# Kernel optimization log

Measured on AMD Instinct MI355X. Metric: run time of the kernel, lower is better.

The kernel has to match this reference:

```python
import jax, jax.numpy as jnp
import numpy as np

CHEB_K = 2; HORIZON = 12; HFS = 4; D_HEAD = 32; EPS = 1e-5

def layer_norm(x, g, b):
    mu = x.mean(-1, keepdims=True)
    v = ((x - mu) ** 2).mean(-1, keepdims=True)
    return (x - mu) * jax.lax.rsqrt(v + EPS) * g + b

def gconv(x, supports, W, b):
    # x:[B,N,C], supports:[K,N,N], W:[N,K,C,O], b:[N,O]
    xg = jnp.einsum('knm,bmc->bnkc', supports, x)
    return jnp.einsum('bnkc,nkco->bno', xg, W) + b

def run_layer(x, state0, supports, gW, gb, uW, ub):
    # x:[B,T,N,C] -> hidden states [B,T,N,H] via GRU-style adaptive graph-conv recurrence
    def step(state, xt):
        xs = jnp.concatenate([xt, state], -1)
        zr = jax.nn.sigmoid(gconv(xs, supports, gW, gb))
        z, r = jnp.split(zr, 2, -1)
        hc = jnp.tanh(gconv(jnp.concatenate([xt, z * state], -1), supports, uW, ub))
        h = r * state + (1.0 - r) * hc
        return h, h
    _, hs = jax.lax.scan(step, state0, x.transpose(1, 0, 2, 3))
    return hs.transpose(1, 0, 2, 3)

def setup_inputs():
    key = jax.random.key(0)
    B, T, N, Din, H, E = 32, 12, 512, 2, 64, 16
    ks = iter(jax.random.split(key, 40))
    def rn(shape, scale):
        return jax.random.normal(next(ks), shape, jnp.float32) * scale
    inp = {}
    inp['source'] = rn((B, T, N, Din), 1.0)
    inp['targets'] = rn((B, T, N, 1), 1.0)
    inp['node_emb'] = rn((N, E), 1.0)
    for l, din in enumerate([Din, H]):
        c = din + H
        inp['gate_wpool_%d' % l] = rn((E, CHEB_K, c, 2 * H), (E * CHEB_K * c) ** -0.5)
        inp['gate_bpool_%d' % l] = rn((E, 2 * H), E ** -0.5)
        inp['upd_wpool_%d' % l] = rn((E, CHEB_K, c, H), (E * CHEB_K * c) ** -0.5)
        inp['upd_bpool_%d' % l] = rn((E, H), E ** -0.5)
    hyp_in = CHEB_K * H * CHEB_K * H
    inp['hyp_W'] = rn((hyp_in, HORIZON * HFS), hyp_in ** -0.5)
    inp['hyp_b'] = rn((HORIZON * HFS,), 0.02)
    for nm in ['Wq', 'Wk', 'Wv', 'ffW1', 'ffW2']:
        inp[nm] = rn((H, H), H ** -0.5)
    for nm in ['bq', 'bk', 'bv', 'ffb1', 'ffb2']:
        inp[nm] = jnp.zeros((H,), jnp.float32)
    inp['ln1_g'] = jnp.ones((H,), jnp.float32); inp['ln1_b'] = jnp.zeros((H,), jnp.float32)
    inp['ln2_g'] = jnp.ones((H,), jnp.float32); inp['ln2_b'] = jnp.zeros((H,), jnp.float32)
    inp['fc_W'] = rn((H, 1), H ** -0.5)
    inp['fc_b'] = jnp.zeros((1,), jnp.float32)
    return inp

def reference(source, targets, node_emb, gate_wpool_0, gate_bpool_0, upd_wpool_0, upd_bpool_0,
              gate_wpool_1, gate_bpool_1, upd_wpool_1, upd_bpool_1, hyp_W, hyp_b,
              Wq, bq, Wk, bk, Wv, bv, ln1_g, ln1_b, ffW1, ffb1, ffW2, ffb2, ln2_g, ln2_b, fc_W, fc_b):
    B, T, N, _ = source.shape
    H = Wq.shape[0]
    # adaptive supports (cheb_k = 2): [I, softmax(relu(E @ E^T), dim=1)]
    adj = jax.nn.softmax(jax.nn.relu(node_emb @ node_emb.T), axis=1)
    supports = jnp.stack([jnp.eye(N, dtype=source.dtype), adj], 0)  # [K,N,N]
    state0 = jnp.zeros((B, N, H), source.dtype)
    out = source
    for (gwp, gbp, uwp, ubp) in [(gate_wpool_0, gate_bpool_0, upd_wpool_0, upd_bpool_0),
                                 (gate_wpool_1, gate_bpool_1, upd_wpool_1, upd_bpool_1)]:
        gW = jnp.einsum('ne,ekio->nkio', node_emb, gwp); gb = node_emb @ gbp
        uW = jnp.einsum('ne,ekio->nkio', node_emb, uwp); ub = node_emb @ ubp
        out = run_layer(out, state0, supports, gW, gb, uW, ub)
        last_uW = uW  # encoder returns last layer's candidate-gconv per-node weights
    # Hypernetwork: dilation=0 grouped 1xHFS conv == scale last hidden state by sum of filter taps
    hlin = last_uW.reshape(N, -1) @ hyp_W + hyp_b               # [N, horizon*HFS]
    fs = hlin.reshape(N, HORIZON, HFS).sum(-1)                  # [N, horizon]
    h = jnp.einsum('bnh,nt->btnh', out[:, -1], fs)              # [B, horizon, N, H]
    # Transform attention block (L = 1; loop re-uses same `out`, only last iter matters)
    heads = H // D_HEAD
    q = out @ Wq + bq; k = out @ Wk + bk; v = h @ Wv + bv
    def split_heads(t):
        return t.reshape(B, T, N, heads, D_HEAD).transpose(3, 0, 2, 1, 4)  # [h,B,N,T,d]
    q, k, v = split_heads(q), split_heads(k), split_heads(v)
    A = jax.nn.softmax(jnp.einsum('hbntd,hbnsd->hbnts', q, k) / (D_HEAD ** 0.5), axis=-1)
    o = jnp.einsum('hbnts,hbnsd->hbntd', A, v)
    o = o.transpose(1, 3, 2, 0, 4).reshape(B, T, N, H)
    val = layer_norm(o + out, ln1_g, ln1_b)
    ffo = jnp.maximum(val @ ffW1 + ffb1, 0.0) @ ffW2 + ffb2
    out_h = layer_norm(ffo + val, ln2_g, ln2_b)
    y = (out_h @ fc_W + fc_b)[..., 0]                           # [B,T,N]
    y = y.reshape(-1, HORIZON, 1, N).transpose(0, 1, 3, 2)      # [B,horizon,N,1]
    return y
```

## Files before the change

### kernel.cpp

```cpp
#include <hip/hip_runtime.h>
#include <hip/hip_bf16.h>


using bf16 = __hip_bfloat16;
#define B2F(x) __bfloat162float(x)

#define NN 512
#define BBATCH 32
#define HHID 64
#define TT 12
#define EE 16

typedef __attribute__((ext_vector_type(4))) float f32x4;
typedef __attribute__((ext_vector_type(8))) short bf16x8;

__device__ inline float wsum(float x) {
#pragma unroll
  for (int off = 32; off > 0; off >>= 1) x += __shfl_xor(x, off, 64);
  return x;
}

__device__ inline uint4 llc_load4(const void* p) {
  uint4 r;
  asm volatile("global_load_dwordx4 %0, %1, off sc0 sc1" : "=v"(r) : "v"(p));
  return r;
}
__device__ inline uint4 cch_load4(const void* p) {
  uint4 r;
  asm volatile("global_load_dwordx4 %0, %1, off" : "=v"(r) : "v"(p));
  return r;
}
__device__ inline uint2 llc_load2(const void* p) {
  uint2 r;
  asm volatile("global_load_dwordx2 %0, %1, off sc0 sc1" : "=v"(r) : "v"(p));
  return r;
}
__device__ inline unsigned llc_load1(const void* p) {
  unsigned r;
  asm volatile("global_load_dword %0, %1, off sc0 sc1" : "=v"(r) : "v"(p));
  return r;
}
__device__ inline void llc_store_bf(void* p, unsigned short v) {
  asm volatile("global_store_short %0, %1, off sc0 sc1" :: "v"(p), "v"((unsigned)v) : "memory");
}
__device__ inline void llc_store_u1(void* p, unsigned v) {
  asm volatile("global_store_dword %0, %1, off sc0 sc1" :: "v"(p), "v"(v) : "memory");
}
template <int N> __device__ inline void wait_vmcnt() {
  if constexpr (N <= 0)      asm volatile("s_waitcnt vmcnt(0)" ::: "memory");
  else if constexpr (N == 1) asm volatile("s_waitcnt vmcnt(1)" ::: "memory");
  else if constexpr (N == 2) asm volatile("s_waitcnt vmcnt(2)" ::: "memory");
  else if constexpr (N == 3) asm volatile("s_waitcnt vmcnt(3)" ::: "memory");
  else if constexpr (N == 4) asm volatile("s_waitcnt vmcnt(4)" ::: "memory");
  else if constexpr (N == 5) asm volatile("s_waitcnt vmcnt(5)" ::: "memory");
  else if constexpr (N == 6) asm volatile("s_waitcnt vmcnt(6)" ::: "memory");
  else if constexpr (N == 7) asm volatile("s_waitcnt vmcnt(7)" ::: "memory");
  else if constexpr (N == 8) asm volatile("s_waitcnt vmcnt(8)" ::: "memory");
  else if constexpr (N == 10) asm volatile("s_waitcnt vmcnt(10)" ::: "memory");
  else if constexpr (N == 12) asm volatile("s_waitcnt vmcnt(12)" ::: "memory");
  else                       asm volatile("s_waitcnt vmcnt(14)" ::: "memory");
}

__device__ inline void lds_barrier() {
  asm volatile("s_waitcnt lgkmcnt(0)" ::: "memory");
  __builtin_amdgcn_s_barrier();
  asm volatile("" ::: "memory");
}

__device__ inline void gbar(unsigned* __restrict__ bar, int& cnt) {
  cnt++;
  __syncthreads();
  unsigned tgt = (unsigned)cnt;
  unsigned* flags = bar + 32;
  if (blockIdx.x == 0) {
    if (threadIdx.x < 64) {
      if (threadIdx.x == 0) llc_store_u1(flags, tgt);
      const unsigned* fp = flags + threadIdx.x * 8;
      bool ok;
      do {
        unsigned v0 = llc_load1(fp + 0), v1 = llc_load1(fp + 1),
                 v2 = llc_load1(fp + 2), v3 = llc_load1(fp + 3),
                 v4 = llc_load1(fp + 4), v5 = llc_load1(fp + 5),
                 v6 = llc_load1(fp + 6), v7 = llc_load1(fp + 7);
        wait_vmcnt<0>();
        __builtin_amdgcn_sched_barrier(0);
        ok = ((int)(v0 - tgt) >= 0) && ((int)(v1 - tgt) >= 0) &&
             ((int)(v2 - tgt) >= 0) && ((int)(v3 - tgt) >= 0) &&
             ((int)(v4 - tgt) >= 0) && ((int)(v5 - tgt) >= 0) &&
             ((int)(v6 - tgt) >= 0) && ((int)(v7 - tgt) >= 0);
      } while (!__all(ok));
      if (threadIdx.x == 0) llc_store_u1(bar, tgt);
    }
  } else if (threadIdx.x == 0) {
    llc_store_u1(flags + blockIdx.x, tgt);
    for (;;) {
      unsigned e = llc_load1(bar);
      wait_vmcnt<0>();
      __builtin_amdgcn_sched_barrier(0);
      if ((int)(e - tgt) >= 0) break;
      __builtin_amdgcn_s_sleep(2);
    }
  }
  __syncthreads();
}

__global__ __launch_bounds__(256) void zero_f32_kernel(float* __restrict__ p, int n) {
  int i = blockIdx.x * 256 + threadIdx.x;
  if (i < n) p[i] = 0.0f;
}


__global__ __launch_bounds__(256) void adj_kernel(const float* __restrict__ emb,
                                                  bf16* __restrict__ adjb) {
  __shared__ float embAll[NN * EE];
  __shared__ float red[256];
  int tid = threadIdx.x, n = blockIdx.x;
  for (int i = tid; i < NN * EE; i += 256) embAll[i] = emb[i];
  __syncthreads();
  float v[2];
#pragma unroll
  for (int j = 0; j < 2; j++) {
    int m = tid + j * 256;
    float s = 0.f;
#pragma unroll
    for (int e = 0; e < EE; e++) s += embAll[n * EE + e] * embAll[m * EE + e];
    v[j] = fmaxf(s, 0.0f);
  }
  float mx = fmaxf(v[0], v[1]);
  red[tid] = mx; __syncthreads();
  for (int s = 128; s > 0; s >>= 1) { if (tid < s) red[tid] = fmaxf(red[tid], red[tid + s]); __syncthreads(); }
  mx = red[0]; __syncthreads();
  float e0 = expf(v[0] - mx), e1 = expf(v[1] - mx);
  red[tid] = e0 + e1; __syncthreads();
  for (int s = 128; s > 0; s >>= 1) { if (tid < s) red[tid] += red[tid + s]; __syncthreads(); }
  float inv = 1.0f / red[0];
  adjb[n * NN + tid] = __float2bfloat16(e0 * inv);
  adjb[n * NN + tid + 256] = __float2bfloat16(e1 * inv);
}

__global__ __launch_bounds__(256) void wgen_kernel(const float* __restrict__ pool,
                                                   const float* __restrict__ emb,
                                                   float* __restrict__ out, int J) {
  __shared__ float embL[128 * EE];
  int tid = threadIdx.x;
  int n0 = blockIdx.y * 128;
  for (int i = tid; i < 128 * EE; i += 256) embL[i] = emb[n0 * EE + i];
  __syncthreads();
  int j = blockIdx.x * 256 + tid;
  if (j >= J) return;
  float pw[EE];
#pragma unroll
  for (int e = 0; e < EE; e++) pw[e] = pool[e * J + j];
#pragma unroll 4
  for (int nn = 0; nn < 128; nn++) {
    float s = 0.f;
#pragma unroll
    for (int e = 0; e < EE; e++) s += embL[nn * EE + e] * pw[e];
    out[(size_t)(n0 + nn) * J + j] = s;
  }
}

__global__ __launch_bounds__(256) void wgen_t_kernel(const float* __restrict__ pool,
                                                     const float* __restrict__ emb,
                                                     bf16* __restrict__ out, int J,
                                                     int O, int KCP, int KC) {
  __shared__ float embL[128 * EE];
  int tid = threadIdx.x;
  int n0 = blockIdx.y * 128;
  for (int i = tid; i < 128 * EE; i += 256) embL[i] = emb[n0 * EE + i];
  __syncthreads();
  int p = blockIdx.x * 256 + tid;
  unsigned kc = (unsigned)p % (unsigned)KCP;
  unsigned o = (unsigned)p / (unsigned)KCP;
  size_t P = (size_t)KCP * O;
  if (kc >= (unsigned)KC) {
    bf16 z = __float2bfloat16(0.f);
    for (int nn = 0; nn < 128; nn++) out[(size_t)(n0 + nn) * P + p] = z;
    return;
  }
  int jp = (int)kc * O + (int)o;
  float pw[EE];
#pragma unroll
  for (int e = 0; e < EE; e++) pw[e] = pool[e * J + jp];
#pragma unroll 4
  for (int nn = 0; nn < 128; nn++) {
    float s = 0.f;
#pragma unroll
    for (int e = 0; e < EE; e++) s += embL[nn * EE + e] * pw[e];
    out[(size_t)(n0 + nn) * P + p] = __float2bfloat16(s);
  }
}

__global__ __launch_bounds__(256) void hypwT_kernel(const float* __restrict__ hypW,
                                                    float* __restrict__ hypWT) {
  __shared__ float tile[48 * 33];
  int r0 = blockIdx.x * 32, tid = threadIdx.x;
  for (int i = tid; i < 32 * 48; i += 256) {
    int r = i / 48, c = i - r * 48;
    tile[c * 33 + r] = hypW[(size_t)(r0 + r) * 48 + c];
  }
  __syncthreads();
  for (int i = tid; i < 48 * 32; i += 256) {
    int c = i >> 5, r = i & 31;
    hypWT[(size_t)c * 16384 + r0 + r] = tile[c * 33 + r];
  }
}

__global__ __launch_bounds__(256) void pw_kernel(const float* __restrict__ upool,
                                                 const float* __restrict__ hypWT,
                                                 float* __restrict__ PW) {
  __shared__ float red[256];
  int j = blockIdx.x, e = blockIdx.y, tid = threadIdx.x;
  float s = 0.f;
#pragma unroll 4
  for (int p = tid; p < 16384; p += 256)
    s += upool[e * 16384 + p] * hypWT[(size_t)j * 16384 + p];
  red[tid] = s; __syncthreads();
  for (int t = 128; t > 0; t >>= 1) { if (tid < t) red[tid] += red[tid + t]; __syncthreads(); }
  if (tid == 0) PW[e * 48 + j] = red[0];
}

__global__ __launch_bounds__(256) void fs_kernel(const float* __restrict__ emb,
                                                 const float* __restrict__ PW,
                                                 const float* __restrict__ hypb,
                                                 float* __restrict__ fs) {
  int id = blockIdx.x * 256 + threadIdx.x;
  if (id >= NN * TT) return;
  int n = id / TT, t = id % TT;
  float s = 0.f;
#pragma unroll
  for (int f = 0; f < 4; f++) {
    int j = t * 4 + f;
    float h = hypb[j];
#pragma unroll
    for (int e = 0; e < EE; e++) h += emb[n * EE + e] * PW[e * 48 + j];
    s += h;
  }
  fs[id] = s;
}

__global__ __launch_bounds__(256) void cvt_src_kernel(const float* __restrict__ src,
                                                      bf16* __restrict__ x) {
  int id = blockIdx.x * 256 + threadIdx.x;
  int c = id & 1, b = (id >> 1) & 31, n = (id >> 6) & 511, t = id >> 15;
  x[id] = __float2bfloat16(src[((b * TT + t) * NN + n) * 2 + c]);
}

#define DBUF 4672

__device__ inline void xsT_wr8(unsigned short* xsT, int base, int q0l, int k, uint4 v) {
  union { uint4 u; unsigned short h[8]; } cv; cv.u = v;
#pragma unroll
  for (int qq = 0; qq < 8; qq++) {
    int q = q0l + qq;
    xsT[base + q * 72 + (q >> 3) * 8 + k] = cv.h[qq];
  }
}

#define DIFF_STEP(cc)                                                         \
  {                                                                           \
    if constexpr ((cc) < 7) {                                                 \
      wait_vmcnt<(6 - (cc)) * LPC>();                                         \
      constexpr int nb = ((((cc) + 1) & 1)) * DBUF;                           \
      xsT_wr8(xsT, nb, ql, kr, pre[((cc) + 1) & 7][0]);                       \
      if constexpr (QW == 64)                                                 \
        xsT_wr8(xsT, nb, ql, 32 + kr, pre[((cc) + 1) & 7][1]);                \
    }                                                                         \
    constexpr int base = ((cc) & 1) * DBUF;                                   \
    _Pragma("unroll")                                                         \
    for (int ki = 0; ki < 2; ki++) {                                          \
      bf16x8 a = apre[(cc) * 2 + ki];                                         \
      _Pragma("unroll")                                                       \
      for (int ct = 0; ct < NCT; ct++) {                                      \
        int q = ct * 16 + col;                                                \
        bf16x8 b = *(const bf16x8*)&xsT[base + q * 72 + (q >> 3) * 8 +        \
                                        ki * 32 + quad * 8];                  \
        acc[ct] = __builtin_amdgcn_mfma_f32_16x16x32_bf16(a, b, acc[ct], 0, 0, 0); \
      }                                                                       \
    }                                                                         \
    lds_barrier();                                                            \
  }

template <int QW, bool CACHED>
__device__ inline void diffuse_tileP(const bf16x8* __restrict__ apre,
                                     const bf16* __restrict__ X, bf16* __restrict__ Y,
                                     int Q, int n0, int q0, char* smraw, int tid) {
  constexpr int LPC = QW / 32;
  constexpr int NCT = QW / 16;
  unsigned short* xsT = (unsigned short*)smraw;
  int w = tid >> 6, lane = tid & 63;
  int col = lane & 15, quad = lane >> 4;
  int kr, ql;
  if constexpr (QW == 64) { kr = tid >> 3; ql = (tid & 7) * 8; }
  else                    { kr = tid >> 2; ql = (tid & 3) * 8; }
  f32x4 acc[NCT];
#pragma unroll
  for (int ct = 0; ct < NCT; ct++) acc[ct] = (f32x4){0.f, 0.f, 0.f, 0.f};
  const bf16* Xb = X + q0 + ql;
  uint4 pre[8][LPC];
#pragma unroll
  for (int c = 0; c < 8; c++) {
    if constexpr (CACHED) {
      pre[c][0] = cch_load4(Xb + (size_t)(c * 64 + kr) * Q);
      if constexpr (QW == 64)
        pre[c][1] = cch_load4(Xb + (size_t)(c * 64 + 32 + kr) * Q);
    } else {
      pre[c][0] = llc_load4(Xb + (size_t)(c * 64 + kr) * Q);
      if constexpr (QW == 64)
        pre[c][1] = llc_load4(Xb + (size_t)(c * 64 + 32 + kr) * Q);
    }
  }
  wait_vmcnt<7 * LPC>();
  xsT_wr8(xsT, 0, ql, kr, pre[0][0]);
  if constexpr (QW == 64) xsT_wr8(xsT, 0, ql, 32 + kr, pre[0][1]);
  lds_barrier();
  DIFF_STEP(0) DIFF_STEP(1) DIFF_STEP(2) DIFF_STEP(3)
  DIFF_STEP(4) DIFF_STEP(5) DIFF_STEP(6) DIFF_STEP(7)
#pragma unroll
  for (int ct = 0; ct < NCT; ct++)
#pragma unroll
    for (int r = 0; r < 4; r++) {
      int row = n0 + w * 16 + quad * 4 + r;
      bf16 hb = __float2bfloat16(acc[ct][r]);
      llc_store_bf(Y + (size_t)row * Q + q0 + ct * 16 + col, *(unsigned short*)&hb);
    }
}


template <int C>
__device__ inline void stage_A(int n, int tid, unsigned short* xinb,
    const bf16* __restrict__ xt, const bf16* __restrict__ xd,
    const bf16* __restrict__ sa, const bf16* __restrict__ sad) {
  constexpr int cc = C + HHID, KC = 2 * cc, KCP = (KC + 31) & ~31, PIT = KCP + 8;
  __syncthreads();
  for (int i = tid; i < 32 * KCP; i += 256) {
    int b = i / KCP, kc = i - b * KCP;
    unsigned short v = 0;
    if (kc < C)            v = *(const unsigned short*)&xt[(n * 32 + b) * C + kc];
    else if (kc < cc)      v = *(const unsigned short*)&sa[(n * 32 + b) * HHID + kc - C];
    else if (kc < cc + C)  v = *(const unsigned short*)&xd[(n * 32 + b) * C + kc - cc];
    else if (kc < KC)      v = *(const unsigned short*)&sad[(n * 32 + b) * HHID + kc - cc - C];
    xinb[b * PIT + kc] = v;
  }
  __syncthreads();
}

template <int C>
__device__ inline void gate_epilogue(int n, int w, int col, int quad,
    f32x4 acc[2][2], const float* __restrict__ gb, const float* __restrict__ state,
    bf16* __restrict__ zs, bf16* __restrict__ rbuf) {
#pragma unroll
  for (int i = 0; i < 2; i++) {
    int o = (w + i * 4) * 16 + col;
    float bv = gb[n * 128 + o];
#pragma unroll
    for (int mt = 0; mt < 2; mt++)
#pragma unroll
      for (int r = 0; r < 4; r++) {
        int m = mt * 16 + quad * 4 + r;
        float zr = 1.0f / (1.0f + expf(-(acc[i][mt][r] + bv)));
        int idx = (n * 32 + m) * HHID + (o & 63);
        if (o < HHID) zs[idx] = __float2bfloat16(zr * state[idx]);
        else          rbuf[idx] = __float2bfloat16(zr);
      }
  }
}

template <int C>
__device__ inline void upd_epilogue(int n, int w, int col, int quad,
    f32x4 acc[2], const float* __restrict__ ub, float* __restrict__ state,
    bf16* __restrict__ sb, const bf16* __restrict__ rbuf, bf16* __restrict__ xo) {
  int o = w * 16 + col;
  float bv = ub[n * 64 + o];
#pragma unroll
  for (int mt = 0; mt < 2; mt++)
#pragma unroll
    for (int r = 0; r < 4; r++) {
      int m = mt * 16 + quad * 4 + r;
      int idx = (n * 32 + m) * HHID + o;
      float hc = tanhf(acc[mt][r] + bv);
      float rr = B2F(rbuf[idx]);
      float st = state[idx];
      float h = rr * st + (1.0f - rr) * hc;
      state[idx] = h;
      bf16 hb = __float2bfloat16(h);
      sb[idx] = hb;
      xo[idx] = hb;
    }
}

template <int C>
__device__ inline void gate_mfma(int n, int tid, const unsigned short* xinb,
    const bf16* __restrict__ gWt, const float* __restrict__ gb,
    const float* __restrict__ state, bf16* __restrict__ zs, bf16* __restrict__ rbuf) {
  constexpr int KC = 2 * (C + HHID), KCP = (KC + 31) & ~31, PIT = KCP + 8;
  int w = tid >> 6, lane = tid & 63, col = lane & 15, quad = lane >> 4;
  f32x4 acc[2][2];
#pragma unroll
  for (int i = 0; i < 2; i++)
#pragma unroll
    for (int mt = 0; mt < 2; mt++) acc[i][mt] = (f32x4){0.f, 0.f, 0.f, 0.f};
  const bf16* Wn = gWt + (size_t)n * KCP * 128;
#pragma unroll 2
  for (int k0 = 0; k0 < KCP; k0 += 32) {
    int ko = k0 + quad * 8;
    bf16x8 a0 = *(const bf16x8*)&xinb[col * PIT + ko];
    bf16x8 a1 = *(const bf16x8*)&xinb[(16 + col) * PIT + ko];
#pragma unroll
    for (int i = 0; i < 2; i++) {
      int o = (w + i * 4) * 16 + col;
      bf16x8 bf = *(const bf16x8*)(Wn + (size_t)o * KCP + ko);
      acc[i][0] = __builtin_amdgcn_mfma_f32_16x16x32_bf16(a0, bf, acc[i][0], 0, 0, 0);
      acc[i][1] = __builtin_amdgcn_mfma_f32_16x16x32_bf16(a1, bf, acc[i][1], 0, 0, 0);
    }
  }
  gate_epilogue<C>(n, w, col, quad, acc, gb, state, zs, rbuf);
}

template <int C>
__device__ inline void upd_mfma(int n, int tid, const unsigned short* xinb,
    const bf16* __restrict__ uWt, const float* __restrict__ ub,
    float* __restrict__ state, bf16* __restrict__ sb,
    const bf16* __restrict__ rbuf, bf16* __restrict__ xo) {
  constexpr int KC = 2 * (C + HHID), KCP = (KC + 31) & ~31, PIT = KCP + 8;
  int w = tid >> 6, lane = tid & 63, col = lane & 15, quad = lane >> 4;
  f32x4 acc[2];
  acc[0] = (f32x4){0.f, 0.f, 0.f, 0.f};
  acc[1] = (f32x4){0.f, 0.f, 0.f, 0.f};
  const bf16* Wn = uWt + (size_t)n * KCP * 64;
  int o = w * 16 + col;
#pragma unroll 2
  for (int k0 = 0; k0 < KCP; k0 += 32) {
    int ko = k0 + quad * 8;
    bf16x8 a0 = *(const bf16x8*)&xinb[col * PIT + ko];
    bf16x8 a1 = *(const bf16x8*)&xinb[(16 + col) * PIT + ko];
    bf16x8 bf = *(const bf16x8*)(Wn + (size_t)o * KCP + ko);
    acc[0] = __builtin_amdgcn_mfma_f32_16x16x32_bf16(a0, bf, acc[0], 0, 0, 0);
    acc[1] = __builtin_amdgcn_mfma_f32_16x16x32_bf16(a1, bf, acc[1], 0, 0, 0);
  }
  upd_epilogue<C>(n, w, col, quad, acc, ub, state, sb, rbuf, xo);
}


template <int C>
__global__ __launch_bounds__(256, 2) void recur_kernel(
    const bf16* __restrict__ adjb, const bf16* __restrict__ xin,
    const bf16* __restrict__ gWt, const float* __restrict__ gb,
    const bf16* __restrict__ uWt, const float* __restrict__ ub,
    bf16* __restrict__ zsAll, bf16* __restrict__ sdiff, bf16* __restrict__ zsdiff,
    bf16* __restrict__ xd, bf16* __restrict__ xout, unsigned* __restrict__ bar) {
  constexpr int KC = 2 * (C + HHID), KCP = (KC + 31) & ~31, PIT = KCP + 8;
  constexpr int NK = KCP / 32;
  constexpr int QX = 32 * C;
  __shared__ __align__(16) char dsm[2 * DBUF * 2];
  __shared__ __align__(16) unsigned short xinb[32 * PIT];
  int bid = blockIdx.x, tid = threadIdx.x;
  int w = tid >> 6, lane = tid & 63, col = lane & 15, quad = lane >> 4;
  int bcnt = 0;

  bf16x8 apre[16];
  {
    int n0p = ((bid & 255) >> 5) * 64;
    const bf16* ar = adjb + (size_t)(n0p + w * 16 + col) * NN;
#pragma unroll
    for (int c = 0; c < 8; c++)
#pragma unroll
      for (int ki = 0; ki < 2; ki++)
        apre[c * 2 + ki] = *(const bf16x8*)(ar + c * 64 + ki * 32 + quad * 8);
  }
  bf16x8 fg[2 * NK];
  {
    const bf16* Wn = gWt + (size_t)bid * KCP * 128;
#pragma unroll
    for (int i = 0; i < 2; i++) {
      int o = (w + i * 4) * 16 + col;
#pragma unroll
      for (int kk = 0; kk < NK; kk++)
        fg[i * NK + kk] = *(const bf16x8*)(Wn + (size_t)o * KCP + kk * 32 + quad * 8);
    }
  }
  bf16x8 fu[NK];
  {
    const bf16* Wn = uWt + (size_t)bid * KCP * 64;
    int o = w * 16 + col;
#pragma unroll
    for (int kk = 0; kk < NK; kk++)
      fu[kk] = *(const bf16x8*)(Wn + (size_t)o * KCP + kk * 32 + quad * 8);
  }
  float gbv0 = gb[bid * 128 + w * 16 + col];
  float gbv1 = gb[bid * 128 + 64 + w * 16 + col];
  float ubv  = ub[bid * 64 + w * 16 + col];

  for (int i = tid; i < 32 * PIT; i += 256) xinb[i] = 0;
  __syncthreads();

  int r2 = tid >> 3, ch = tid & 7;
  uint4 vxt; unsigned sxt = 0, sxd = 0;
  if constexpr (C == 64) {
    vxt = *(const uint4*)(xin + (size_t)(bid * 32 + r2) * 64 + ch * 8);
  } else {
    if (tid < 32) sxt = *(const unsigned*)(xin + (size_t)(bid * 32 + tid) * 2);
  }

  float st[2][4], rr_[2][4];
#pragma unroll
  for (int mt = 0; mt < 2; mt++)
#pragma unroll
    for (int r4 = 0; r4 < 4; r4++) st[mt][r4] = 0.f;

  if constexpr (C == 2) {
    int wg = (bid & 31) | ((bid >> 8) << 5);
    if (wg < TT)
      diffuse_tileP<64, true>(apre, xin + (size_t)wg * NN * QX,
                              xd + (size_t)wg * NN * QX, QX,
                              ((bid & 255) >> 5) * 64, 0, dsm, tid);
  } else {
    if (bid >= 256)
      diffuse_tileP<64, true>(apre, xin, xd, 2048, ((bid & 255) >> 5) * 64,
                              (bid & 31) * 64, dsm, tid);
  }
  gbar(bar, bcnt);

  for (int t = 0; t < TT; t++) {
    const bf16* xt = xin + (size_t)t * NN * QX;
    const bf16* xdt = (C == 2) ? (xd + (size_t)t * NN * QX) : xd;
    bf16* xo = xout + (size_t)t * NN * 32 * HHID;
    bf16* zst = zsAll + (size_t)t * NN * 32 * HHID;
    if (t > 0) {
      const bf16* sbp = xout + (size_t)(t - 1) * NN * 32 * HHID;
      if constexpr (C == 64) {
        if (bid < 256)
          diffuse_tileP<64, true>(apre, sbp, sdiff, 2048, (bid >> 5) * 64,
                                  (bid & 31) * 64, dsm, tid);
        else
          diffuse_tileP<64, true>(apre, xt, xd, 2048, ((bid & 255) >> 5) * 64,
                                  (bid & 31) * 64, dsm, tid);
      } else {
        int cs = (bid & 31) | ((bid >> 8) << 5);
        diffuse_tileP<32, true>(apre, sbp, sdiff, 2048, ((bid & 255) >> 5) * 64,
                                cs * 32, dsm, tid);
      }
      gbar(bar, bcnt);
    }
    if constexpr (C == 64) {
      *(uint4*)&xinb[r2 * PIT + ch * 8] = vxt;
      uint4 v1 = llc_load4(xdt + (size_t)(bid * 32 + r2) * 64 + ch * 8);
      uint4 v2;
      if (t > 0) v2 = llc_load4(sdiff + (size_t)(bid * 32 + r2) * 64 + ch * 8);
      wait_vmcnt<0>();
      *(uint4*)&xinb[r2 * PIT + 128 + ch * 8] = v1;
      if (t > 0) *(uint4*)&xinb[r2 * PIT + 192 + ch * 8] = v2;
    } else {
      if (tid < 32) *(unsigned*)&xinb[tid * PIT] = sxt;
      if (t == 0) {
        if (tid < 32) {
          unsigned v = llc_load1(xdt + (size_t)(bid * 32 + tid) * 2);
          wait_vmcnt<0>();
          *(unsigned*)&xinb[tid * PIT + 66] = v;
        }
      } else {
        if (tid >= 32 && tid < 64) *(unsigned*)&xinb[(tid - 32) * PIT + 66] = sxd;
        int r2a = tid >> 4, c4 = tid & 15;
        uint2 va = llc_load2(sdiff + (size_t)(bid * 32 + r2a) * 64 + c4 * 4);
        uint2 vb = llc_load2(sdiff + (size_t)(bid * 32 + 16 + r2a) * 64 + c4 * 4);
        wait_vmcnt<0>();
        *(uint2*)&xinb[r2a * PIT + 68 + c4 * 4] = va;
        *(uint2*)&xinb[(16 + r2a) * PIT + 68 + c4 * 4] = vb;
      }
    }
    __syncthreads();
    {
      f32x4 acc[2][2];
#pragma unroll
      for (int i = 0; i < 2; i++)
#pragma unroll
        for (int mt = 0; mt < 2; mt++) acc[i][mt] = (f32x4){0.f, 0.f, 0.f, 0.f};
#pragma unroll
      for (int kk = 0; kk < NK; kk++) {
        int ko = kk * 32 + quad * 8;
        bf16x8 a0 = *(const bf16x8*)&xinb[col * PIT + ko];
        bf16x8 a1 = *(const bf16x8*)&xinb[(16 + col) * PIT + ko];
#pragma unroll
        for (int i = 0; i < 2; i++) {
          acc[i][0] = __builtin_amdgcn_mfma_f32_16x16x32_bf16(a0, fg[i * NK + kk], acc[i][0], 0, 0, 0);
          acc[i][1] = __builtin_amdgcn_mfma_f32_16x16x32_bf16(a1, fg[i * NK + kk], acc[i][1], 0, 0, 0);
        }
      }
      __syncthreads();
#pragma unroll
      for (int mt = 0; mt < 2; mt++)
#pragma unroll
        for (int r4 = 0; r4 < 4; r4++) {
          int m = mt * 16 + quad * 4 + r4;
          float z = 1.0f / (1.0f + expf(-(acc[0][mt][r4] + gbv0)));
          float rv = 1.0f / (1.0f + expf(-(acc[1][mt][r4] + gbv1)));
          rr_[mt][r4] = rv;
          bf16 zb = __float2bfloat16(z * st[mt][r4]);
          xinb[m * PIT + C + w * 16 + col] = *(unsigned short*)&zb;
          llc_store_bf(zst + (size_t)(bid * 32 + m) * 64 + w * 16 + col,
                       *(unsigned short*)&zb);
        }
    }
    if (t > 0) {
      gbar(bar, bcnt);
      {
        int cs = (bid & 31) | ((bid >> 8) << 5);
        diffuse_tileP<32, true>(apre, zst, zsdiff, 2048, ((bid & 255) >> 5) * 64,
                                cs * 32, dsm, tid);
      }
      gbar(bar, bcnt);
      if constexpr (C == 64) {
        uint4 v = llc_load4(zsdiff + (size_t)(bid * 32 + r2) * 64 + ch * 8);
        wait_vmcnt<0>();
        *(uint4*)&xinb[r2 * PIT + 192 + ch * 8] = v;
      } else {
        int r2a = tid >> 4, c4 = tid & 15;
        uint2 va = llc_load2(zsdiff + (size_t)(bid * 32 + r2a) * 64 + c4 * 4);
        uint2 vb = llc_load2(zsdiff + (size_t)(bid * 32 + 16 + r2a) * 64 + c4 * 4);
        wait_vmcnt<0>();
        *(uint2*)&xinb[r2a * PIT + 68 + c4 * 4] = va;
        *(uint2*)&xinb[(16 + r2a) * PIT + 68 + c4 * 4] = vb;
      }
    }
    __syncthreads();
    {
      f32x4 acc[2];
      acc[0] = (f32x4){0.f, 0.f, 0.f, 0.f};
      acc[1] = (f32x4){0.f, 0.f, 0.f, 0.f};
#pragma unroll
      for (int kk = 0; kk < NK; kk++) {
        int ko = kk * 32 + quad * 8;
        bf16x8 a0 = *(const bf16x8*)&xinb[col * PIT + ko];
        bf16x8 a1 = *(const bf16x8*)&xinb[(16 + col) * PIT + ko];
        acc[0] = __builtin_amdgcn_mfma_f32_16x16x32_bf16(a0, fu[kk], acc[0], 0, 0, 0);
        acc[1] = __builtin_amdgcn_mfma_f32_16x16x32_bf16(a1, fu[kk], acc[1], 0, 0, 0);
      }
      __syncthreads();
      if (t + 1 < TT) {
        if constexpr (C == 64) {
          vxt = *(const uint4*)(xin + (size_t)(t + 1) * NN * QX +
                                (size_t)(bid * 32 + r2) * 64 + ch * 8);
        } else {
          if (tid < 32)
            sxt = *(const unsigned*)(xin + (size_t)(t + 1) * NN * QX +
                                     (size_t)(bid * 32 + tid) * 2);
          else if (tid < 64)
            sxd = *(const unsigned*)(xd + (size_t)(t + 1) * NN * QX +
                                     (size_t)(bid * 32 + (tid - 32)) * 2);
        }
      }
#pragma unroll
      for (int mt = 0; mt < 2; mt++)
#pragma unroll
        for (int r4 = 0; r4 < 4; r4++) {
          int m = mt * 16 + quad * 4 + r4;
          float hc = tanhf(acc[mt][r4] + ubv);
          float rv = rr_[mt][r4];
          float h = rv * st[mt][r4] + (1.0f - rv) * hc;
          st[mt][r4] = h;
          bf16 hb = __float2bfloat16(h);
          xinb[m * PIT + C + w * 16 + col] = *(unsigned short*)&hb;
          llc_store_bf(xo + (size_t)(bid * 32 + m) * 64 + w * 16 + col,
                       *(unsigned short*)&hb);
        }
    }
    gbar(bar, bcnt);
  }
}


__global__ __launch_bounds__(256, 2) void diffuse0_kernel(const bf16* __restrict__ adjb,
                                                          const bf16* __restrict__ X,
                                                          bf16* __restrict__ Y) {
  __shared__ __align__(16) char smraw[2 * DBUF * 2];
  int bid = blockIdx.x, tid = threadIdx.x;
  int t = bid >> 3, n0 = (bid & 7) * 64;
  int w = tid >> 6, lane = tid & 63, col = lane & 15, quad = lane >> 4;
  bf16x8 ap[16];
  const bf16* ar = adjb + (size_t)(n0 + w * 16 + col) * NN;
#pragma unroll
  for (int c = 0; c < 8; c++)
#pragma unroll
    for (int ki = 0; ki < 2; ki++)
      ap[c * 2 + ki] = *(const bf16x8*)(ar + c * 64 + ki * 32 + quad * 8);
  diffuse_tileP<64, true>(ap, X + (size_t)t * NN * 64, Y + (size_t)t * NN * 64,
                          64, n0, 0, smraw, tid);
}

__global__ __launch_bounds__(256, 2) void diffuse1_kernel(const bf16* __restrict__ adjb,
                                                          const bf16* __restrict__ X,
                                                          bf16* __restrict__ Y) {
  __shared__ __align__(16) char smraw[2 * DBUF * 2];
  int bid = blockIdx.x, tid = threadIdx.x;
  int n0 = (bid >> 5) * 64;
  int w = tid >> 6, lane = tid & 63, col = lane & 15, quad = lane >> 4;
  bf16x8 ap[16];
  const bf16* ar = adjb + (size_t)(n0 + w * 16 + col) * NN;
#pragma unroll
  for (int c = 0; c < 8; c++)
#pragma unroll
    for (int ki = 0; ki < 2; ki++)
      ap[c * 2 + ki] = *(const bf16x8*)(ar + c * 64 + ki * 32 + quad * 8);
  diffuse_tileP<64, true>(ap, X, Y, 2048, n0, (bid & 31) * 64, smraw, tid);
}

template <int C>
__global__ __launch_bounds__(256, 2) void gate_wrap(
    const bf16* xt, const bf16* xdt, const bf16* sa, const bf16* sad,
    const bf16* gWt, const float* gb, const float* state, bf16* zs, bf16* rbuf) {
  constexpr int KC = 2 * (C + HHID), KCP = (KC + 31) & ~31, PIT = KCP + 8;
  __shared__ __align__(16) unsigned short xinb[32 * PIT];
  stage_A<C>(blockIdx.x, threadIdx.x, xinb, xt, xdt, sa, sad);
  gate_mfma<C>(blockIdx.x, threadIdx.x, xinb, gWt, gb, state, zs, rbuf);
}

template <int C>
__global__ __launch_bounds__(256, 2) void upd_wrap(
    const bf16* xt, const bf16* xdt, const bf16* sa, const bf16* sad,
    const bf16* uWt, const float* ub, float* state, bf16* sb,
    const bf16* rbuf, bf16* xo) {
  constexpr int KC = 2 * (C + HHID), KCP = (KC + 31) & ~31, PIT = KCP + 8;
  __shared__ __align__(16) unsigned short xinb[32 * PIT];
  stage_A<C>(blockIdx.x, threadIdx.x, xinb, xt, xdt, sa, sad);
  upd_mfma<C>(blockIdx.x, threadIdx.x, xinb, uWt, ub, state, sb, rbuf, xo);
}


#define TP 68
#define WS 72

__global__ __launch_bounds__(256, 4) void attn1_kernel(
    const bf16* __restrict__ x1, const float* __restrict__ fsb,
    const float* __restrict__ Wq, const float* __restrict__ bq,
    const float* __restrict__ Wk, const float* __restrict__ bk,
    const float* __restrict__ Wv, const float* __restrict__ bv,
    const float* __restrict__ ln1g, const float* __restrict__ ln1b,
    bf16* __restrict__ val) {
  __shared__ bf16 WqT[WS * 64], WkT[WS * 64];
  __shared__ bf16 Wv_s[4096];
  __shared__ bf16 Xb[16 * 72];
  __shared__ float qs[TT * TP], ks[TT * TP];
  __shared__ float A[2 * TT * TT];
  __shared__ float ovv[64], fss[TT];
  __shared__ float bqs[64], bks[64], bvs[64], g1s[64], b1s[64];
  int tid = threadIdx.x;
  int w = tid >> 6, lane = tid & 63, col = lane & 15, quad = lane >> 4;
#pragma unroll
  for (int i = 0; i < 16; i++) {
    int e = tid * 16 + i;
    int hi = e >> 6, ho = e & 63;
    WqT[ho * WS + hi] = __float2bfloat16(Wq[e]);
    WkT[ho * WS + hi] = __float2bfloat16(Wk[e]);
  }
  for (int i = tid; i < 4096; i += 256) Wv_s[i] = __float2bfloat16(Wv[i]);
  for (int i = tid; i < 16 * 72; i += 256) Xb[i] = __float2bfloat16(0.f);
  if (tid < 64) {
    bqs[tid] = bq[tid]; bks[tid] = bk[tid]; bvs[tid] = bv[tid];
    g1s[tid] = ln1g[tid]; b1s[tid] = ln1b[tid];
  }
  __syncthreads();
  for (int g = 0; g < 8; g++) {
    int p = blockIdx.x * 8 + g;
    int b = p >> 9, n = p & 511;
    for (int i = tid; i < TT * 64; i += 256) {
      int t = i >> 6, j = i & 63;
      Xb[t * 72 + j] = x1[(((size_t)t * NN + n) * BBATCH + b) * HHID + j];
    }
    if (tid < TT) fss[tid] = fsb[n * TT + tid];
    __syncthreads();
    {
      f32x4 aq = (f32x4){0.f, 0.f, 0.f, 0.f};
      f32x4 ak = (f32x4){0.f, 0.f, 0.f, 0.f};
#pragma unroll
      for (int ki = 0; ki < 2; ki++) {
        bf16x8 af = *(const bf16x8*)&Xb[col * 72 + ki * 32 + quad * 8];
        bf16x8 bqf = *(const bf16x8*)&WqT[(w * 16 + col) * WS + ki * 32 + quad * 8];
        bf16x8 bkf = *(const bf16x8*)&WkT[(w * 16 + col) * WS + ki * 32 + quad * 8];
        aq = __builtin_amdgcn_mfma_f32_16x16x32_bf16(af, bqf, aq, 0, 0, 0);
        ak = __builtin_amdgcn_mfma_f32_16x16x32_bf16(af, bkf, ak, 0, 0, 0);
      }
#pragma unroll
      for (int r = 0; r < 4; r++) {
        int t = quad * 4 + r;
        if (t < TT) {
          int h = w * 16 + col;
          qs[t * TP + h] = aq[r] + bqs[h];
          ks[t * TP + h] = ak[r] + bks[h];
        }
      }
    }
    if (tid < 64) {
      float s = 0.f;
#pragma unroll 8
      for (int j = 0; j < 64; j++)
        s += B2F(Xb[11 * 72 + j]) * B2F(Wv_s[j * 64 + tid]);
      ovv[tid] = s;
    }
    __syncthreads();
    for (int i = tid; i < 2 * TT * TT; i += 256) {
      int hd = i / (TT * TT), ts = i % (TT * TT), t = ts / TT, s = ts % TT;
      float acc = 0.f;
#pragma unroll
      for (int d = 0; d < 32; d++) acc += qs[t * TP + hd * 32 + d] * ks[s * TP + hd * 32 + d];
      A[i] = acc * 0.17677669529663687f;
    }
    __syncthreads();
    if (tid < 2 * TT) {
      int hd = tid / TT, t = tid % TT;
      float* row = &A[hd * TT * TT + t * TT];
      float m = row[0];
      for (int s = 1; s < TT; s++) m = fmaxf(m, row[s]);
      float sm = 0.f;
      for (int s = 0; s < TT; s++) { float e = expf(row[s] - m); row[s] = e; sm += e; }
      float inv = 1.0f / sm;
      for (int s = 0; s < TT; s++) row[s] *= inv;
    }
    __syncthreads();
#pragma unroll
    for (int it = 0; it < 3; it++) {
      int i = it * 256 + tid;
      int t = i >> 6, h = i & 63, hd = h >> 5;
      float afs = 0.f;
#pragma unroll
      for (int s = 0; s < TT; s++) afs += A[hd * TT * TT + t * TT + s] * fss[s];
      float o = ovv[h] * afs + bvs[h];
      float x = o + B2F(Xb[t * 72 + h]);
      float mu = wsum(x) * (1.0f / 64.0f);
      float d = x - mu;
      float var = wsum(d * d) * (1.0f / 64.0f);
      float v = d * rsqrtf(var + 1e-5f) * g1s[h] + b1s[h];
      val[((size_t)(b * TT + t) * NN + n) * HHID + h] = __float2bfloat16(v);
    }
    __syncthreads();
  }
}

__global__ __launch_bounds__(256, 4) void ffn_kernel(
    const bf16* __restrict__ val, const float* __restrict__ W1, const float* __restrict__ b1,
    const float* __restrict__ W2, const float* __restrict__ b2,
    const float* __restrict__ ln2g, const float* __restrict__ ln2b,
    const float* __restrict__ fcW, const float* __restrict__ fcb,
    float* __restrict__ out, int rows_per_block) {
  __shared__ bf16 W1T[WS * 64], W2T[WS * 64];
  __shared__ bf16 Ab[16 * 72];
  __shared__ bf16 Hh[16 * 72], Hl[16 * 72];
  __shared__ float fout[16 * 68];
  __shared__ float b1s[64], b2s[64], g2s[64], bb2[64], fcs[64];
  int tid = threadIdx.x;
  int w = tid >> 6, lane = tid & 63, col = lane & 15, quad = lane >> 4;
#pragma unroll
  for (int i = 0; i < 16; i++) {
    int e = tid * 16 + i;
    int hi = e >> 6, ho = e & 63;
    W1T[ho * WS + hi] = __float2bfloat16(W1[e]);
    W2T[ho * WS + hi] = __float2bfloat16(W2[e]);
  }
  if (tid < 64) {
    b1s[tid] = b1[tid]; b2s[tid] = b2[tid];
    g2s[tid] = ln2g[tid]; bb2[tid] = ln2b[tid]; fcs[tid] = fcW[tid];
  }
  __syncthreads();
  float fcbv = fcb[0];
  for (int c0 = 0; c0 < rows_per_block; c0 += 16) {
    size_t r0 = (size_t)blockIdx.x * rows_per_block + c0;
    for (int i = tid; i < 1024; i += 256) {
      int rr = i >> 6, j = i & 63;
      Ab[rr * 72 + j] = val[(r0 + rr) * 64 + j];
    }
    __syncthreads();
    {
      f32x4 a1 = (f32x4){0.f, 0.f, 0.f, 0.f};
#pragma unroll
      for (int ki = 0; ki < 2; ki++) {
        bf16x8 af = *(const bf16x8*)&Ab[col * 72 + ki * 32 + quad * 8];
        bf16x8 bf1 = *(const bf16x8*)&W1T[(w * 16 + col) * WS + ki * 32 + quad * 8];
        a1 = __builtin_amdgcn_mfma_f32_16x16x32_bf16(af, bf1, a1, 0, 0, 0);
      }
#pragma unroll
      for (int r = 0; r < 4; r++) {
        int m = quad * 4 + r, h = w * 16 + col;
        float hv = fmaxf(a1[r] + b1s[h], 0.0f);
        bf16 hb = __float2bfloat16(hv);
        float lo = hv - B2F(hb);
        Hh[m * 72 + h] = hb;
        Hl[m * 72 + h] = __float2bfloat16(lo);
      }
    }
    __syncthreads();
    {
      f32x4 a2 = (f32x4){0.f, 0.f, 0.f, 0.f};
#pragma unroll
      for (int ki = 0; ki < 2; ki++) {
        bf16x8 ah = *(const bf16x8*)&Hh[col * 72 + ki * 32 + quad * 8];
        bf16x8 al = *(const bf16x8*)&Hl[col * 72 + ki * 32 + quad * 8];
        bf16x8 bf2 = *(const bf16x8*)&W2T[(w * 16 + col) * WS + ki * 32 + quad * 8];
        a2 = __builtin_amdgcn_mfma_f32_16x16x32_bf16(ah, bf2, a2, 0, 0, 0);
        a2 = __builtin_amdgcn_mfma_f32_16x16x32_bf16(al, bf2, a2, 0, 0, 0);
      }
#pragma unroll
      for (int r = 0; r < 4; r++) {
        int m = quad * 4 + r, h = w * 16 + col;
        fout[m * 68 + h] = a2[r] + b2s[h] + B2F(Ab[m * 72 + h]);
      }
    }
    __syncthreads();
#pragma unroll
    for (int p4 = 0; p4 < 4; p4++) {
      int m = p4 * 4 + w;
      float y = fout[m * 68 + lane];
      float mu = wsum(y) * (1.0f / 64.0f);
      float d = y - mu;
      float var = wsum(d * d) * (1.0f / 64.0f);
      float oh = d * rsqrtf(var + 1e-5f) * g2s[lane] + bb2[lane];
      float contrib = wsum(oh * fcs[lane]);
      if (lane == 0) out[r0 + m] = contrib + fcbv;
    }
    __syncthreads();
  }
}

extern "C" void kernel_launch(void* const* d_in, const int* in_sizes, int n_in,
                              void* d_out, int out_size, void* d_ws, size_t ws_size,
                              hipStream_t stream) {
  const float* src = (const float*)d_in[0];
  const float* emb = (const float*)d_in[2];
  const float* gwp[2] = {(const float*)d_in[3], (const float*)d_in[7]};
  const float* gbp[2] = {(const float*)d_in[4], (const float*)d_in[8]};
  const float* uwp[2] = {(const float*)d_in[5], (const float*)d_in[9]};
  const float* ubp[2] = {(const float*)d_in[6], (const float*)d_in[10]};
  const float* hypW = (const float*)d_in[11];
  const float* hypb = (const float*)d_in[12];
  const float *Wq, *Wk, *Wv, *ffW1, *ffW2, *bq, *bk, *bv, *ffb1, *ffb2;
  const float *ln1g, *ln1b, *ln2g, *ln2b, *fcW, *fcb;
  if (in_sizes[14] == 4096) {
    Wq = (const float*)d_in[13]; Wk = (const float*)d_in[14]; Wv = (const float*)d_in[15];
    ffW1 = (const float*)d_in[16]; ffW2 = (const float*)d_in[17];
    bq = (const float*)d_in[18]; bk = (const float*)d_in[19]; bv = (const float*)d_in[20];
    ffb1 = (const float*)d_in[21]; ffb2 = (const float*)d_in[22];
    ln1g = (const float*)d_in[23]; ln1b = (const float*)d_in[24];
    ln2g = (const float*)d_in[25]; ln2b = (const float*)d_in[26];
    fcW = (const float*)d_in[27]; fcb = (const float*)d_in[28];
  } else {
    Wq = (const float*)d_in[13]; bq = (const float*)d_in[14];
    Wk = (const float*)d_in[15]; bk = (const float*)d_in[16];
    Wv = (const float*)d_in[17]; bv = (const float*)d_in[18];
    ln1g = (const float*)d_in[19]; ln1b = (const float*)d_in[20];
    ffW1 = (const float*)d_in[21]; ffb1 = (const float*)d_in[22];
    ffW2 = (const float*)d_in[23]; ffb2 = (const float*)d_in[24];
    ln2g = (const float*)d_in[25]; ln2b = (const float*)d_in[26];
    fcW = (const float*)d_in[27]; fcb = (const float*)d_in[28];
  }
  float* outp = (float*)d_out;

  char* ws = (char*)d_ws;
  size_t off = 0;
  auto alloc = [&](size_t bytes) {
    void* p = ws + off;
    off += (bytes + 255) & ~(size_t)255;
    return p;
  };
  bf16* adjb = (bf16*)alloc((size_t)512 * 512 * 2);
  bf16* gWb = (bf16*)alloc((size_t)512 * 32768 * 2);
  bf16* uWb = (bf16*)alloc((size_t)512 * 16384 * 2);
  float* gb = (float*)alloc((size_t)512 * 128 * 4);
  float* ub = (float*)alloc((size_t)512 * 64 * 4);
  bf16* xin0 = (bf16*)alloc((size_t)12 * 512 * 32 * 2 * 2);
  bf16* x0 = (bf16*)alloc((size_t)12 * 512 * 32 * 64 * 2);
  bf16* xout1 = (bf16*)alloc((size_t)12 * 512 * 32 * 64 * 2);
  bf16* xd0 = (bf16*)alloc((size_t)12 * 512 * 32 * 2 * 2);
  bf16* xdL1 = (bf16*)alloc((size_t)512 * 32 * 64 * 2);
  float* state = (float*)alloc((size_t)512 * 32 * 64 * 4);
  bf16* sb = (bf16*)alloc((size_t)512 * 32 * 64 * 2);
  bf16* sdiff = (bf16*)alloc((size_t)512 * 32 * 64 * 2);
  bf16* zsAll = (bf16*)alloc((size_t)12 * 512 * 32 * 64 * 2);
  bf16* zsdiff = (bf16*)alloc((size_t)512 * 32 * 64 * 2);
  bf16* rbuf = (bf16*)alloc((size_t)512 * 32 * 64 * 2);
  float* PW = (float*)alloc((size_t)16 * 48 * 4);
  float* fsb = (float*)alloc((size_t)512 * 12 * 4);
  unsigned* bar = (unsigned*)alloc((size_t)544 * 4);
  float* hypWT = (float*)alloc((size_t)48 * 16384 * 4);
  bf16* val = gWb;

  adj_kernel<<<512, 256, 0, stream>>>(emb, adjb);
  hypwT_kernel<<<512, 256, 0, stream>>>(hypW, hypWT);
  pw_kernel<<<dim3(48, 16), 256, 0, stream>>>(uwp[1], hypWT, PW);
  fs_kernel<<<24, 256, 0, stream>>>(emb, PW, hypb, fsb);
  cvt_src_kernel<<<1536, 256, 0, stream>>>(src, xin0);

  int occ0 = 0, occ1 = 0;
  hipOccupancyMaxActiveBlocksPerMultiprocessor(&occ0, recur_kernel<2>, 256, 0);
  hipOccupancyMaxActiveBlocksPerMultiprocessor(&occ1, recur_kernel<64>, 256, 0);

  for (int l = 0; l < 2; l++) {
    int C = (l == 0) ? 2 : 64;
    int KC = 2 * (C + 64);
    int KCP = (KC + 31) & ~31;
    int JG = KC * 128, JU = KC * 64;
    wgen_t_kernel<<<dim3(KCP * 128 / 256, 4), 256, 0, stream>>>(
        gwp[l], emb, gWb, JG, 128, KCP, KC);
    wgen_t_kernel<<<dim3(KCP * 64 / 256, 4), 256, 0, stream>>>(
        uwp[l], emb, uWb, JU, 64, KCP, KC);
    wgen_kernel<<<dim3(1, 4), 256, 0, stream>>>(gbp[l], emb, gb, 128);
    wgen_kernel<<<dim3(1, 4), 256, 0, stream>>>(ubp[l], emb, ub, 64);
    zero_f32_kernel<<<3, 256, 0, stream>>>((float*)bar, 544);

    const bf16* xin = (l == 0) ? xin0 : x0;
    bf16* xout_l = (l == 0) ? x0 : xout1;
    bf16* xd = (l == 0) ? xd0 : xdL1;
    int occ = (l == 0) ? occ0 : occ1;
    if (occ >= 2) {
      if (l == 0)
        recur_kernel<2><<<512, 256, 0, stream>>>(adjb, xin, gWb, gb, uWb, ub,
                                                 zsAll, sdiff, zsdiff, xd, xout_l, bar);
      else
        recur_kernel<64><<<512, 256, 0, stream>>>(adjb, xin, gWb, gb, uWb, ub,
                                                  zsAll, sdiff, zsdiff, xd, xout_l, bar);
    } else {
      zero_f32_kernel<<<4096, 256, 0, stream>>>(state, 512 * 32 * 64);
      zero_f32_kernel<<<2048, 256, 0, stream>>>((float*)sb, 512 * 32 * 64 / 2);
      if (l == 0) diffuse0_kernel<<<96, 256, 0, stream>>>(adjb, xin, xd);
      for (int t = 0; t < 12; t++) {
        const bf16* xt = xin + (size_t)t * 512 * 32 * C;
        const bf16* xdt = (l == 0) ? (xd + (size_t)t * 512 * 32 * C) : xd;
        bf16* xo = xout_l + (size_t)t * 512 * 32 * 64;
        if (l == 1) diffuse1_kernel<<<256, 256, 0, stream>>>(adjb, xt, xd);
        diffuse1_kernel<<<256, 256, 0, stream>>>(adjb, sb, sdiff);
        if (l == 0)
          gate_wrap<2><<<512, 256, 0, stream>>>(xt, xdt, sb, sdiff, gWb, gb, state, zsAll, rbuf);
        else
          gate_wrap<64><<<512, 256, 0, stream>>>(xt, xdt, sb, sdiff, gWb, gb, state, zsAll, rbuf);
        diffuse1_kernel<<<256, 256, 0, stream>>>(adjb, zsAll, zsdiff);
        if (l == 0)
          upd_wrap<2><<<512, 256, 0, stream>>>(xt, xdt, zsAll, zsdiff, uWb, ub, state, sb, rbuf, xo);
        else
          upd_wrap<64><<<512, 256, 0, stream>>>(xt, xdt, zsAll, zsdiff, uWb, ub, state, sb, rbuf, xo);
      }
    }
  }

  attn1_kernel<<<2048, 256, 0, stream>>>(xout1, fsb, Wq, bq, Wk, bk, Wv, bv, ln1g, ln1b, val);
  ffn_kernel<<<2048, 256, 0, stream>>>(val, ffW1, ffb1, ffW2, ffb2, ln2g, ln2b, fcW, fcb,
                                       outp, 96);
}
```

Baseline: 1.637 ms.

## Fuse attention and FFN epilogue kernels, pretransposing bf16 weights once

Merges the attention/LN1 kernel and the FFN/LN2/fc kernel into one kernel, so each (b,n) group's 12 LN1 rows stay in shared memory instead of going through a global bf16 buffer. A small pre-kernel converts and transposes Wq, Wk, Wv, W1 and W2 to bf16 once. The fused kernel then reads them from global/L2 instead of every block building its own shared copies. The Wv projection is also split across all four waves with a partial-sum reduction. The cost is MFMA B-operand loads from global memory rather than LDS, and only 12 of 16 rows per tile are used in the FFN.

```diff
diff --git a/kernel.cpp b/kernel.cpp
--- a/kernel.cpp
+++ b/kernel.cpp
@@ -244,6 +244,20 @@
   int id = blockIdx.x * 256 + threadIdx.x;
   int c = id & 1, b = (id >> 1) & 31, n = (id >> 6) & 511, t = id >> 15;
   x[id] = __float2bfloat16(src[((b * TT + t) * NN + n) * 2 + c]);
+}
+
+__global__ __launch_bounds__(256) void epiW_kernel(
+    const float* __restrict__ Wq, const float* __restrict__ Wk,
+    const float* __restrict__ Wv, const float* __restrict__ W1,
+    const float* __restrict__ W2, bf16* __restrict__ wb) {
+  int e = blockIdx.x * 256 + threadIdx.x;
+  int hi = e >> 6, ho = e & 63;
+  int et = ho * 64 + hi;
+  wb[et] = __float2bfloat16(Wq[e]);
+  wb[4096 + et] = __float2bfloat16(Wk[e]);
+  wb[8192 + e] = __float2bfloat16(Wv[e]);
+  wb[12288 + et] = __float2bfloat16(W1[e]);
+  wb[16384 + et] = __float2bfloat16(W2[e]);
 }
 
 #define DBUF 4672
@@ -727,38 +741,46 @@
 
 
 #define TP 68
-#define WS 72
-
-__global__ __launch_bounds__(256, 4) void attn1_kernel(
+
+__global__ __launch_bounds__(256, 4) void attn_ffn_kernel(
     const bf16* __restrict__ x1, const float* __restrict__ fsb,
-    const float* __restrict__ Wq, const float* __restrict__ bq,
-    const float* __restrict__ Wk, const float* __restrict__ bk,
-    const float* __restrict__ Wv, const float* __restrict__ bv,
+    const bf16* __restrict__ wb,
+    const float* __restrict__ bq, const float* __restrict__ bk,
+    const float* __restrict__ bv,
     const float* __restrict__ ln1g, const float* __restrict__ ln1b,
-    bf16* __restrict__ val) {
-  __shared__ bf16 WqT[WS * 64], WkT[WS * 64];
-  __shared__ bf16 Wv_s[4096];
+    const float* __restrict__ ffb1, const float* __restrict__ ffb2,
+    const float* __restrict__ ln2g, const float* __restrict__ ln2b,
+    const float* __restrict__ fcW, const float* __restrict__ fcb,
+    float* __restrict__ out) {
+  const bf16* WqT = wb;
+  const bf16* WkT = wb + 4096;
+  const bf16* Wvb = wb + 8192;
+  const bf16* W1T = wb + 12288;
+  const bf16* W2T = wb + 16384;
   __shared__ bf16 Xb[16 * 72];
+  __shared__ bf16 vrows[16 * 72];
+  __shared__ bf16 Hh[16 * 72], Hl[16 * 72];
   __shared__ float qs[TT * TP], ks[TT * TP];
   __shared__ float A[2 * TT * TT];
+  __shared__ float fout[16 * 68];
+  __shared__ float vpart[4 * 64];
   __shared__ float ovv[64], fss[TT];
   __shared__ float bqs[64], bks[64], bvs[64], g1s[64], b1s[64];
+  __shared__ float b1f[64], b2f[64], g2s[64], bb2[64], fcs[64];
   int tid = threadIdx.x;
   int w = tid >> 6, lane = tid & 63, col = lane & 15, quad = lane >> 4;
-#pragma unroll
-  for (int i = 0; i < 16; i++) {
-    int e = tid * 16 + i;
-    int hi = e >> 6, ho = e & 63;
-    WqT[ho * WS + hi] = __float2bfloat16(Wq[e]);
-    WkT[ho * WS + hi] = __float2bfloat16(Wk[e]);
-  }
-  for (int i = tid; i < 4096; i += 256) Wv_s[i] = __float2bfloat16(Wv[i]);
-  for (int i = tid; i < 16 * 72; i += 256) Xb[i] = __float2bfloat16(0.f);
+  for (int i = tid; i < 16 * 72; i += 256) {
+    Xb[i] = __float2bfloat16(0.f);
+    vrows[i] = __float2bfloat16(0.f);
+  }
   if (tid < 64) {
     bqs[tid] = bq[tid]; bks[tid] = bk[tid]; bvs[tid] = bv[tid];
     g1s[tid] = ln1g[tid]; b1s[tid] = ln1b[tid];
+    b1f[tid] = ffb1[tid]; b2f[tid] = ffb2[tid];
+    g2s[tid] = ln2g[tid]; bb2[tid] = ln2b[tid]; fcs[tid] = fcW[tid];
   }
   __syncthreads();
+  float fcbv = fcb[0];
   for (int g = 0; g < 8; g++) {
     int p = blockIdx.x * 8 + g;
     int b = p >> 9, n = p & 511;
@@ -774,8 +796,8 @@
 #pragma unroll
       for (int ki = 0; ki < 2; ki++) {
         bf16x8 af = *(const bf16x8*)&Xb[col * 72 + ki * 32 + quad * 8];
-        bf16x8 bqf = *(const bf16x8*)&WqT[(w * 16 + col) * WS + ki * 32 + quad * 8];
-        bf16x8 bkf = *(const bf16x8*)&WkT[(w * 16 + col) * WS + ki * 32 + quad * 8];
+        bf16x8 bqf = *(const bf16x8*)&WqT[(w * 16 + col) * 64 + ki * 32 + quad * 8];
+        bf16x8 bkf = *(const bf16x8*)&WkT[(w * 16 + col) * 64 + ki * 32 + quad * 8];
         aq = __builtin_amdgcn_mfma_f32_16x16x32_bf16(af, bqf, aq, 0, 0, 0);
         ak = __builtin_amdgcn_mfma_f32_16x16x32_bf16(af, bkf, ak, 0, 0, 0);
       }
@@ -789,14 +811,17 @@
         }
       }
     }
-    if (tid < 64) {
+    {
+      int h = tid & 63, gq = tid >> 6;
       float s = 0.f;
-#pragma unroll 8
-      for (int j = 0; j < 64; j++)
-        s += B2F(Xb[11 * 72 + j]) * B2F(Wv_s[j * 64 + tid]);
-      ovv[tid] = s;
+#pragma unroll
+      for (int j = 0; j < 16; j++)
+        s += B2F(Xb[11 * 72 + gq * 16 + j]) * B2F(Wvb[(gq * 16 + j) * 64 + h]);
+      vpart[gq * 64 + h] = s;
     }
     __syncthreads();
+    if (tid < 64)
+      ovv[tid] = vpart[tid] + vpart[64 + tid] + vpart[128 + tid] + vpart[192 + tid];
     for (int i = tid; i < 2 * TT * TT; i += 256) {
       int hd = i / (TT * TT), ts = i % (TT * TT), t = ts / TT, s = ts % TT;
       float acc = 0.f;
@@ -829,57 +854,21 @@
       float d = x - mu;
       float var = wsum(d * d) * (1.0f / 64.0f);
       float v = d * rsqrtf(var + 1e-5f) * g1s[h] + b1s[h];
-      val[((size_t)(b * TT + t) * NN + n) * HHID + h] = __float2bfloat16(v);
-    }
-    __syncthreads();
-  }
-}
-
-__global__ __launch_bounds__(256, 4) void ffn_kernel(
-    const bf16* __restrict__ val, const float* __restrict__ W1, const float* __restrict__ b1,
-    const float* __restrict__ W2, const float* __restrict__ b2,
-    const float* __restrict__ ln2g, const float* __restrict__ ln2b,
-    const float* __restrict__ fcW, const float* __restrict__ fcb,
-    float* __restrict__ out, int rows_per_block) {
-  __shared__ bf16 W1T[WS * 64], W2T[WS * 64];
-  __shared__ bf16 Ab[16 * 72];
-  __shared__ bf16 Hh[16 * 72], Hl[16 * 72];
-  __shared__ float fout[16 * 68];
-  __shared__ float b1s[64], b2s[64], g2s[64], bb2[64], fcs[64];
-  int tid = threadIdx.x;
-  int w = tid >> 6, lane = tid & 63, col = lane & 15, quad = lane >> 4;
-#pragma unroll
-  for (int i = 0; i < 16; i++) {
-    int e = tid * 16 + i;
-    int hi = e >> 6, ho = e & 63;
-    W1T[ho * WS + hi] = __float2bfloat16(W1[e]);
-    W2T[ho * WS + hi] = __float2bfloat16(W2[e]);
-  }
-  if (tid < 64) {
-    b1s[tid] = b1[tid]; b2s[tid] = b2[tid];
-    g2s[tid] = ln2g[tid]; bb2[tid] = ln2b[tid]; fcs[tid] = fcW[tid];
-  }
-  __syncthreads();
-  float fcbv = fcb[0];
-  for (int c0 = 0; c0 < rows_per_block; c0 += 16) {
-    size_t r0 = (size_t)blockIdx.x * rows_per_block + c0;
-    for (int i = tid; i < 1024; i += 256) {
-      int rr = i >> 6, j = i & 63;
-      Ab[rr * 72 + j] = val[(r0 + rr) * 64 + j];
+      vrows[t * 72 + h] = __float2bfloat16(v);
     }
     __syncthreads();
     {
       f32x4 a1 = (f32x4){0.f, 0.f, 0.f, 0.f};
 #pragma unroll
       for (int ki = 0; ki < 2; ki++) {
-        bf16x8 af = *(const bf16x8*)&Ab[col * 72 + ki * 32 + quad * 8];
-        bf16x8 bf1 = *(const bf16x8*)&W1T[(w * 16 + col) * WS + ki * 32 + quad * 8];
+        bf16x8 af = *(const bf16x8*)&vrows[col * 72 + ki * 32 + quad * 8];
+        bf16x8 bf1 = *(const bf16x8*)&W1T[(w * 16 + col) * 64 + ki * 32 + quad * 8];
         a1 = __builtin_amdgcn_mfma_f32_16x16x32_bf16(af, bf1, a1, 0, 0, 0);
       }
 #pragma unroll
       for (int r = 0; r < 4; r++) {
         int m = quad * 4 + r, h = w * 16 + col;
-        float hv = fmaxf(a1[r] + b1s[h], 0.0f);
+        float hv = fmaxf(a1[r] + b1f[h], 0.0f);
         bf16 hb = __float2bfloat16(hv);
         float lo = hv - B2F(hb);
         Hh[m * 72 + h] = hb;
@@ -893,19 +882,19 @@
       for (int ki = 0; ki < 2; ki++) {
         bf16x8 ah = *(const bf16x8*)&Hh[col * 72 + ki * 32 + quad * 8];
         bf16x8 al = *(const bf16x8*)&Hl[col * 72 + ki * 32 + quad * 8];
-        bf16x8 bf2 = *(const bf16x8*)&W2T[(w * 16 + col) * WS + ki * 32 + quad * 8];
+        bf16x8 bf2 = *(const bf16x8*)&W2T[(w * 16 + col) * 64 + ki * 32 + quad * 8];
         a2 = __builtin_amdgcn_mfma_f32_16x16x32_bf16(ah, bf2, a2, 0, 0, 0);
         a2 = __builtin_amdgcn_mfma_f32_16x16x32_bf16(al, bf2, a2, 0, 0, 0);
       }
 #pragma unroll
       for (int r = 0; r < 4; r++) {
         int m = quad * 4 + r, h = w * 16 + col;
-        fout[m * 68 + h] = a2[r] + b2s[h] + B2F(Ab[m * 72 + h]);
+        fout[m * 68 + h] = a2[r] + b2f[h] + B2F(vrows[m * 72 + h]);
       }
     }
     __syncthreads();
 #pragma unroll
-    for (int p4 = 0; p4 < 4; p4++) {
+    for (int p4 = 0; p4 < 3; p4++) {
       int m = p4 * 4 + w;
       float y = fout[m * 68 + lane];
       float mu = wsum(y) * (1.0f / 64.0f);
@@ -913,7 +902,7 @@
       float var = wsum(d * d) * (1.0f / 64.0f);
       float oh = d * rsqrtf(var + 1e-5f) * g2s[lane] + bb2[lane];
       float contrib = wsum(oh * fcs[lane]);
-      if (lane == 0) out[r0 + m] = contrib + fcbv;
+      if (lane == 0) out[((size_t)b * TT + m) * NN + n] = contrib + fcbv;
     }
     __syncthreads();
   }
@@ -979,13 +968,14 @@
   float* fsb = (float*)alloc((size_t)512 * 12 * 4);
   unsigned* bar = (unsigned*)alloc((size_t)544 * 4);
   float* hypWT = (float*)alloc((size_t)48 * 16384 * 4);
-  bf16* val = gWb;
+  bf16* epiW = (bf16*)alloc((size_t)5 * 4096 * 2);
 
   adj_kernel<<<512, 256, 0, stream>>>(emb, adjb);
   hypwT_kernel<<<512, 256, 0, stream>>>(hypW, hypWT);
   pw_kernel<<<dim3(48, 16), 256, 0, stream>>>(uwp[1], hypWT, PW);
   fs_kernel<<<24, 256, 0, stream>>>(emb, PW, hypb, fsb);
   cvt_src_kernel<<<1536, 256, 0, stream>>>(src, xin0);
+  epiW_kernel<<<16, 256, 0, stream>>>(Wq, Wk, Wv, ffW1, ffW2, epiW);
 
   int occ0 = 0, occ1 = 0;
   hipOccupancyMaxActiveBlocksPerMultiprocessor(&occ0, recur_kernel<2>, 256, 0);
@@ -1038,7 +1028,7 @@
     }
   }
 
-  attn1_kernel<<<2048, 256, 0, stream>>>(xout1, fsb, Wq, bq, Wk, bk, Wv, bv, ln1g, ln1b, val);
-  ffn_kernel<<<2048, 256, 0, stream>>>(val, ffW1, ffb1, ffW2, ffb2, ln2g, ln2b, fcW, fcb,
-                                       outp, 96);
-}
+  attn_ffn_kernel<<<2048, 256, 0, stream>>>(
+      xout1, fsb, epiW, bq, bk, bv, ln1g, ln1b, ffb1, ffb2, ln2g, ln2b,
+      fcW, fcb, outp);
+}
```

Measured after the change: 1.701 ms. 1.04x slower.
